# Kernel optimization log

Hardware: AMD Instinct MI355X
Metric: run time of the kernel (lower is better)

Reference implementation:

```python
import jax, jax.numpy as jnp
import numpy as np

T = 262144        # sequence_length
K = 512           # num_basis
DEGREE = 3
EPS = 1e-6


def setup_inputs() -> dict:
    # Deterministic buffers, matching the torch module's __init__ exactly.
    t = jnp.linspace(-1.0, 1.0, T, dtype=jnp.float32)
    num_knots = K + DEGREE + 1
    inner = jnp.linspace(-1.0, 1.0, num_knots - 2 * DEGREE, dtype=jnp.float32)
    knots = jnp.concatenate([
        jnp.full((DEGREE,), -1.0, dtype=jnp.float32),
        inner,
        jnp.full((DEGREE,), 1.0, dtype=jnp.float32),
    ])
    return {"t": t, "knots": knots}


def _bspline(t, kv):
    n0 = K + DEGREE  # number of degree-0 basis functions
    tc = t[:, None]  # [T, 1]
    # degree-0: indicator of [kv[i], kv[i+1]) ; last interval is closed.
    cond1 = tc >= kv[None, :n0]
    cond2 = tc < kv[None, 1:n0 + 1]
    last_closed = tc <= kv[None, n0:n0 + 1]
    cond2 = jnp.concatenate([cond2[:, :-1], last_closed], axis=1)
    bases = (cond1 & cond2).astype(t.dtype)  # [T, K+DEGREE]
    # Cox-de Boor recursion, vectorized over knot index i.
    for d in range(1, DEGREE + 1):
        n = K + DEGREE - d
        den1 = kv[d:d + n] - kv[:n]            # [n]
        den2 = kv[d + 1:d + n + 1] - kv[1:n + 1]
        c1 = jnp.where(den1 >= EPS, (tc - kv[None, :n]) / jnp.where(den1 >= EPS, den1, 1.0), 0.0)
        c2 = jnp.where(den2 >= EPS, (kv[None, d + 1:d + n + 1] - tc) / jnp.where(den2 >= EPS, den2, 1.0), 0.0)
        bases = c1 * bases[:, :n] + c2 * bases[:, 1:n + 1]
    return bases  # [T, K]


def reference(t, knots):
    return _bspline(t, knots)
```

## Files before the change

### kernel.cpp

```cpp
#include <hip/hip_runtime.h>


namespace {
constexpr int K_N  = 512;
constexpr int NKN  = 516;
constexpr int DEG  = 3;
constexpr float EPSF = 1e-6f;
constexpr int ROWS = 16;
constexpr int BLK  = 256;
}

__global__ __launch_bounds__(BLK)
void bspline_basis_kernel(const float* __restrict__ t_arr,
                          const float* __restrict__ knots,
                          float* __restrict__ out)
{
    __shared__ float kv[NKN];
    __shared__ float vals[ROWS][4];
    __shared__ int   j0s[ROWS];

    const int tid = threadIdx.x;
    for (int i = tid; i < NKN; i += BLK) kv[i] = knots[i];
    __syncthreads();

    const int row_base = blockIdx.x * ROWS;

    if (tid < ROWS) {
        const float t = t_arr[row_base + tid];
        int j0 = -16;
        float N0 = 0.f, N1 = 0.f, N2 = 0.f, N3 = 0.f;
        if (t < kv[K_N]) {
            int lo = DEG, hi = K_N - 1;
            while (lo < hi) {
                const int mid = (lo + hi + 1) >> 1;
                if (t >= kv[mid]) lo = mid; else hi = mid - 1;
            }
            const int s = lo;
            float N[4] = {1.f, 0.f, 0.f, 0.f};
            #pragma unroll
            for (int d = 1; d <= DEG; ++d) {
                float nn[4];
                #pragma unroll
                for (int k = 0; k <= d; ++k) {
                    const int j = s - d + k;
                    const float left  = (k >= 1)     ? N[k - 1] : 0.f;
                    const float right = (k <= d - 1) ? N[k]     : 0.f;
                    const float den1 = kv[j + d]     - kv[j];
                    const float den2 = kv[j + d + 1] - kv[j + 1];
                    const float c1 = (den1 >= EPSF) ? (t - kv[j]) / den1 : 0.f;
                    const float c2 = (den2 >= EPSF) ? (kv[j + d + 1] - t) / den2 : 0.f;
                    nn[k] = c1 * left + c2 * right;
                }
                #pragma unroll
                for (int k = 0; k <= d; ++k) N[k] = nn[k];
            }
            j0 = s - DEG;
            N0 = N[0]; N1 = N[1]; N2 = N[2]; N3 = N[3];
        }
        j0s[tid] = j0;
        vals[tid][0] = N0; vals[tid][1] = N1;
        vals[tid][2] = N2; vals[tid][3] = N3;
    }
    __syncthreads();

    float4* out4 = reinterpret_cast<float4*>(out + (size_t)row_base * K_N);
    constexpr int TOTAL_F4 = ROWS * (K_N / 4);
    #pragma unroll
    for (int it = 0; it < TOTAL_F4 / BLK; ++it) {
        const int idx = it * BLK + tid;
        const int r   = idx >> 7;
        const int c   = (idx & 127) << 2;
        const int j0  = j0s[r];
        float e[4];
        #pragma unroll
        for (int k = 0; k < 4; ++k) {
            const int rel = c + k - j0;
            const float v = vals[r][rel & 3];
            e[k] = (rel >= 0 && rel <= 3) ? v : 0.f;
        }
        out4[idx] = make_float4(e[0], e[1], e[2], e[3]);
    }
}

extern "C" void kernel_launch(void* const* d_in, const int* in_sizes, int n_in,
                              void* d_out, int out_size, void* d_ws, size_t ws_size,
                              hipStream_t stream) {
    const float* t_arr = (const float*)d_in[0];
    const float* knots = (const float*)d_in[1];
    float* out = (float*)d_out;
    const int n_rows = in_sizes[0];
    dim3 grid(n_rows / ROWS);
    hipLaunchKernelGGL(bspline_basis_kernel, grid, dim3(BLK), 0, stream,
                       t_arr, knots, out);
}
```

Baseline: 520.2 us.

## Replace dense tile writes with memset plus per-row sparse scatter of nonzeros

The fused kernel that wrote every output element, mostly zeros, is split into a hipMemsetAsync that zeroes the whole output and a kernel where each thread evaluates one row and writes only its four nonzero basis values. The aim is to let the driver's fill path handle the large zero write and to remove the shared-memory staging and the mostly idle compute threads. In exchange the four per-row stores are uncoalesced and land on lines the memset has already written, which adds a second launch and extra write traffic.

After: 545.0 us. +4.8%, slower.

```diff
diff --git a/kernel.cpp b/kernel.cpp
--- a/kernel.cpp
+++ b/kernel.cpp
@@ -6,80 +6,52 @@
 constexpr int NKN  = 516;
 constexpr int DEG  = 3;
 constexpr float EPSF = 1e-6f;
-constexpr int ROWS = 16;
 constexpr int BLK  = 256;
 }
 
 __global__ __launch_bounds__(BLK)
-void bspline_basis_kernel(const float* __restrict__ t_arr,
-                          const float* __restrict__ knots,
-                          float* __restrict__ out)
+void bspline_scatter_kernel(const float* __restrict__ t_arr,
+                            const float* __restrict__ knots,
+                            float* __restrict__ out, int n_rows)
 {
     __shared__ float kv[NKN];
-    __shared__ float vals[ROWS][4];
-    __shared__ int   j0s[ROWS];
-
-    const int tid = threadIdx.x;
-    for (int i = tid; i < NKN; i += BLK) kv[i] = knots[i];
+    for (int i = threadIdx.x; i < NKN; i += BLK) kv[i] = knots[i];
     __syncthreads();
 
-    const int row_base = blockIdx.x * ROWS;
+    const int row = blockIdx.x * BLK + threadIdx.x;
+    if (row >= n_rows) return;
+    const float t = t_arr[row];
 
-    if (tid < ROWS) {
-        const float t = t_arr[row_base + tid];
-        int j0 = -16;
-        float N0 = 0.f, N1 = 0.f, N2 = 0.f, N3 = 0.f;
-        if (t < kv[K_N]) {
-            int lo = DEG, hi = K_N - 1;
-            while (lo < hi) {
-                const int mid = (lo + hi + 1) >> 1;
-                if (t >= kv[mid]) lo = mid; else hi = mid - 1;
-            }
-            const int s = lo;
-            float N[4] = {1.f, 0.f, 0.f, 0.f};
-            #pragma unroll
-            for (int d = 1; d <= DEG; ++d) {
-                float nn[4];
-                #pragma unroll
-                for (int k = 0; k <= d; ++k) {
-                    const int j = s - d + k;
-                    const float left  = (k >= 1)     ? N[k - 1] : 0.f;
-                    const float right = (k <= d - 1) ? N[k]     : 0.f;
-                    const float den1 = kv[j + d]     - kv[j];
-                    const float den2 = kv[j + d + 1] - kv[j + 1];
-                    const float c1 = (den1 >= EPSF) ? (t - kv[j]) / den1 : 0.f;
-                    const float c2 = (den2 >= EPSF) ? (kv[j + d + 1] - t) / den2 : 0.f;
-                    nn[k] = c1 * left + c2 * right;
-                }
-                #pragma unroll
-                for (int k = 0; k <= d; ++k) N[k] = nn[k];
-            }
-            j0 = s - DEG;
-            N0 = N[0]; N1 = N[1]; N2 = N[2]; N3 = N[3];
+    if (!(t < kv[K_N])) return;
+
+    int lo = DEG, hi = K_N - 1;
+    while (lo < hi) {
+        const int mid = (lo + hi + 1) >> 1;
+        if (t >= kv[mid]) lo = mid; else hi = mid - 1;
+    }
+    const int s = lo;
+
+    float N[4] = {1.f, 0.f, 0.f, 0.f};
+    #pragma unroll
+    for (int d = 1; d <= DEG; ++d) {
+        float nn[4];
+        #pragma unroll
+        for (int k = 0; k <= d; ++k) {
+            const int j = s - d + k;
+            const float left  = (k >= 1)     ? N[k - 1] : 0.f;
+            const float right = (k <= d - 1) ? N[k]     : 0.f;
+            const float den1 = kv[j + d]     - kv[j];
+            const float den2 = kv[j + d + 1] - kv[j + 1];
+            const float c1 = (den1 >= EPSF) ? (t - kv[j]) / den1 : 0.f;
+            const float c2 = (den2 >= EPSF) ? (kv[j + d + 1] - t) / den2 : 0.f;
+            nn[k] = c1 * left + c2 * right;
         }
-        j0s[tid] = j0;
-        vals[tid][0] = N0; vals[tid][1] = N1;
-        vals[tid][2] = N2; vals[tid][3] = N3;
+        #pragma unroll
+        for (int k = 0; k <= d; ++k) N[k] = nn[k];
     }
-    __syncthreads();
 
-    float4* out4 = reinterpret_cast<float4*>(out + (size_t)row_base * K_N);
-    constexpr int TOTAL_F4 = ROWS * (K_N / 4);
-    #pragma unroll
-    for (int it = 0; it < TOTAL_F4 / BLK; ++it) {
-        const int idx = it * BLK + tid;
-        const int r   = idx >> 7;
-        const int c   = (idx & 127) << 2;
-        const int j0  = j0s[r];
-        float e[4];
-        #pragma unroll
-        for (int k = 0; k < 4; ++k) {
-            const int rel = c + k - j0;
-            const float v = vals[r][rel & 3];
-            e[k] = (rel >= 0 && rel <= 3) ? v : 0.f;
-        }
-        out4[idx] = make_float4(e[0], e[1], e[2], e[3]);
-    }
+    float* p = out + (size_t)row * K_N + (s - DEG);
+    p[0] = N[0]; p[1] = N[1]; p[2] = N[2]; p[3] = N[3];
 }
 
 extern "C" void kernel_launch(void* const* d_in, const int* in_sizes, int n_in,
@@ -89,7 +61,10 @@
     const float* knots = (const float*)d_in[1];
     float* out = (float*)d_out;
     const int n_rows = in_sizes[0];
-    dim3 grid(n_rows / ROWS);
-    hipLaunchKernelGGL(bspline_basis_kernel, grid, dim3(BLK), 0, stream,
-                       t_arr, knots, out);
+
+    hipMemsetAsync(out, 0, (size_t)n_rows * K_N * sizeof(float), stream);
+
+    dim3 grid((n_rows + BLK - 1) / BLK);
+    hipLaunchKernelGGL(bspline_scatter_kernel, grid, dim3(BLK), 0, stream,
+                       t_arr, knots, out, n_rows);
 }
```
